# Kernel tuning notes

Measured on AMD Instinct MI355X. Metric: run time of the kernel, lower is better.

The kernel has to match this reference:

```python
import jax, jax.numpy as jnp
import numpy as np
import math

EPS = float(jnp.finfo(jnp.float32).eps)


def _mask_imag(z, n_ops):
    # Zero the imaginary part of (b,c) slices whose relative imaginary
    # magnitude is below the FFT roundoff threshold (vectorized version of
    # the original per-(i,j) Python loop).
    re, im = z.real, z.imag
    max_im = jnp.max(jnp.abs(im), axis=(-2, -1), keepdims=True)
    max_abs = jnp.max(jnp.abs(z), axis=(-2, -1), keepdims=True)
    mask = (max_im / max_abs) <= (n_ops * EPS)
    im = jnp.where(mask, jnp.zeros_like(im), im)
    return jax.lax.complex(re, im)


def otf2psf(otf, outsize):
    h, w = otf.shape[-2], otf.shape[-1]
    n_ops = h * w * (math.log2(h) + math.log2(w))
    psf = jnp.fft.ifft2(otf)
    psf = _mask_imag(psf, n_ops)
    psf = jnp.roll(psf, (outsize[0] // 2, outsize[1] // 2), axis=(-2, -1))
    return psf[..., : outsize[0], : outsize[1]]


def psf2otf(psf, shape):
    p0, p1 = psf.shape[-2], psf.shape[-1]
    n_ops = p0 * p1 * (math.log2(p0) + math.log2(p1))
    pad = [(0, 0)] * (psf.ndim - 2) + [(0, shape[0] - p0), (0, shape[1] - p1)]
    otf = jnp.pad(psf, pad)
    otf = jnp.roll(otf, (-(p0 // 2), -(p1 // 2)), axis=(-2, -1))
    otf = jnp.fft.fft2(otf)
    return _mask_imag(otf, n_ops)


def compute_ax(psf, latent_ft, image_size, psf_size_2d, gamma):
    xf = psf2otf(psf, image_size)          # [b, cp, H, W] complex
    y = jnp.real(otf2psf(latent_ft * xf, psf_size_2d))  # [b, c, p, p]
    return y + gamma * psf


def conjgrad(x, latent_ft, b_rhs, n_iter, image_size, psf_size_2d, gamma):
    r = b_rhs - compute_ax(x, latent_ft, image_size, psf_size_2d, gamma)
    p = r
    rsold = jnp.sum(r * r, axis=(-2, -1), keepdims=True)
    for _ in range(n_iter):  # small fixed iteration count
        Ap = compute_ax(p, latent_ft, image_size, psf_size_2d, gamma)
        alpha = rsold / jnp.sum(p * Ap, axis=(-2, -1), keepdims=True)
        x = x + alpha * p
        r = r - alpha * Ap
        rsnew = jnp.sum(r * r, axis=(-2, -1), keepdims=True)
        p = r + (rsnew / rsold) * p
        rsold = rsnew
    return x


def setup_inputs() -> dict:
    key = jax.random.key(0)
    k1, k2, k3, k4 = jax.random.split(key, 4)
    shape = (4, 3, 512, 512)
    return {
        "blurx": jax.random.normal(k1, shape, dtype=jnp.float32),
        "blury": jax.random.normal(k2, shape, dtype=jnp.float32),
        "latentx": jax.random.normal(k3, shape, dtype=jnp.float32),
        "latenty": jax.random.normal(k4, shape, dtype=jnp.float32),
        "psf_size": 31,
    }


def reference(blurx, blury, latentx, latenty, psf_size):
    n_iter = 10
    gamma = 1.0
    blur = jnp.sqrt(blurx ** 2 + blury ** 2)
    latent = jnp.sqrt(latentx ** 2 + latenty ** 2)
    b, c, h, w = blur.shape
    kernel = jnp.full((b, 1, psf_size, psf_size), 1.0 / float(psf_size ** 2), dtype=blur.dtype)
    blur_f = jnp.fft.fft2(blur)
    latent_f = jnp.fft.fft2(latent)
    bf = jnp.conj(latent_f) * blur_f
    latent_ft = jnp.conj(latent_f) * latent_f
    blur_otf = jnp.real(otf2psf(bf, (psf_size, psf_size)))  # [b, c, p, p]
    kernel = conjgrad(kernel, latent_ft, blur_otf, n_iter, (h, w), (psf_size, psf_size), gamma)
    # threshold small entries, clamp negatives, normalize
    kf = kernel.reshape(b, c, -1)
    max_var = jnp.max(kf, axis=2, keepdims=True)
    kf = jnp.where(kf < 0.05 * max_var, jnp.zeros_like(kf), kf)
    kernel = kf.reshape(b, c, psf_size, psf_size)
    kernel = jnp.where(kernel < 0, jnp.zeros_like(kernel), kernel)
    kernel = kernel / jnp.sum(kernel, axis=(-2, -1), keepdims=True)
    return kernel
```

## Files before the change

### kernel.cpp

```cpp
#include <hip/hip_runtime.h>
#include <math.h>

#define NIMG 12
#define NN 512
#define NPIX (NN * NN)
#define XST (257 * 512)

__device__ __forceinline__ int brev9(int p) {
  return (int)(__brev((unsigned)p) >> 23);
}

__device__ __forceinline__ void fft512_core(
    float vr[8], float vi[8], const int inv,
    const float* __restrict__ twr, const float* __restrict__ twi,
    const int lane)
{
#pragma unroll
  for (int s = 0; s < 3; ++s) {
    const int half = 1 << s;
#pragma unroll
    for (int e = 0; e < 8; ++e) {
      if ((e & half) == 0) {
        const int j = (e & (half - 1)) << (8 - s);
        const float wr = twr[j];
        const float wi = inv ? -twi[j] : twi[j];
        const float br = vr[e + half], bi = vi[e + half];
        const float tr = __fsub_rn(__fmul_rn(wr, br), __fmul_rn(wi, bi));
        const float ti = __fadd_rn(__fmul_rn(wr, bi), __fmul_rn(wi, br));
        vr[e + half] = __fsub_rn(vr[e], tr); vi[e + half] = __fsub_rn(vi[e], ti);
        vr[e] = __fadd_rn(vr[e], tr); vi[e] = __fadd_rn(vi[e], ti);
      }
    }
  }
#pragma unroll
  for (int s = 3; s <= 8; ++s) {
    const int xm = 1 << (s - 3);
    const bool low = (lane & xm) == 0;
#pragma unroll
    for (int e = 0; e < 8; ++e) {
      const float orr = __shfl_xor(vr[e], xm);
      const float oii = __shfl_xor(vi[e], xm);
      const int j = ((((lane & (xm - 1)) << 3) | e)) << (8 - s);
      const float wr = twr[j];
      const float wi = inv ? -twi[j] : twi[j];
      if (low) {
        const float tr = __fsub_rn(__fmul_rn(wr, orr), __fmul_rn(wi, oii));
        const float ti = __fadd_rn(__fmul_rn(wr, oii), __fmul_rn(wi, orr));
        vr[e] = __fadd_rn(vr[e], tr); vi[e] = __fadd_rn(vi[e], ti);
      } else {
        const float tr = __fsub_rn(__fmul_rn(wr, vr[e]), __fmul_rn(wi, vi[e]));
        const float ti = __fadd_rn(__fmul_rn(wr, vi[e]), __fmul_rn(wi, vr[e]));
        vr[e] = __fsub_rn(orr, tr); vi[e] = __fsub_rn(oii, ti);
      }
    }
  }
  if (inv) {
    const float sc = 1.0f / 512.0f;
#pragma unroll
    for (int e = 0; e < 8; ++e) {
      vr[e] = __fmul_rn(vr[e], sc); vi[e] = __fmul_rn(vi[e], sc);
    }
  }
}

__device__ __forceinline__ float np_pw_base(const float* a, int n)
{
  float r0 = a[0], r1 = a[1], r2 = a[2], r3 = a[3];
  float r4 = a[4], r5 = a[5], r6 = a[6], r7 = a[7];
  int i = 8;
  const int lim = n - (n & 7);
  for (; i < lim; i += 8) {
    r0 = __fadd_rn(r0, a[i + 0]); r1 = __fadd_rn(r1, a[i + 1]);
    r2 = __fadd_rn(r2, a[i + 2]); r3 = __fadd_rn(r3, a[i + 3]);
    r4 = __fadd_rn(r4, a[i + 4]); r5 = __fadd_rn(r5, a[i + 5]);
    r6 = __fadd_rn(r6, a[i + 6]); r7 = __fadd_rn(r7, a[i + 7]);
  }
  float res = __fadd_rn(
      __fadd_rn(__fadd_rn(r0, r1), __fadd_rn(r2, r3)),
      __fadd_rn(__fadd_rn(r4, r5), __fadd_rn(r6, r7)));
  for (; i < n; ++i) res = __fadd_rn(res, a[i]);
  return res;
}

__global__ __launch_bounds__(256) void twiddle_kernel(float2* __restrict__ twg)
{
  const int k = threadIdx.x;
  double s, c;
  sincos(-2.0 * M_PI * (double)k / 512.0, &s, &c);
  twg[k] = make_float2((float)c, (float)s);
}

__global__ __launch_bounds__(256) void loadmag_kernel(
    const float* __restrict__ bx, const float* __restrict__ by,
    const float* __restrict__ lx, const float* __restrict__ ly,
    float2* __restrict__ B2, float2* __restrict__ B1)
{
  const int i = blockIdx.x * 256 + threadIdx.x;
  {
    const float a = lx[i], b = ly[i];
    const float s = __fadd_rn(__fmul_rn(a, a), __fmul_rn(b, b));
    B2[i] = make_float2((float)sqrt((double)s), 0.f);
  }
  {
    const float a = bx[i], b = by[i];
    const float s = __fadd_rn(__fmul_rn(a, a), __fmul_rn(b, b));
    B1[i] = make_float2((float)sqrt((double)s), 0.f);
  }
}

__global__ __launch_bounds__(256) void rowfft_kernel(
    float2* __restrict__ A, float2* __restrict__ B,
    const float2* __restrict__ twg)
{
  __shared__ float twr[256], twi[256];
  { const float2 t = twg[threadIdx.x]; twr[threadIdx.x] = t.x; twi[threadIdx.x] = t.y; }
  __syncthreads();
  int wid = blockIdx.x * 4 + (threadIdx.x >> 6);
  const int lane = threadIdx.x & 63;
  float2* buf = A;
  if (wid >= NIMG * NN) { wid -= NIMG * NN; buf = B; }
  const int base = (wid >> 9) * NPIX + (wid & 511) * NN;
  float vr[8], vi[8];
#pragma unroll
  for (int e = 0; e < 8; ++e) {
    const float2 z = buf[base + brev9(lane * 8 + e)];
    vr[e] = z.x; vi[e] = z.y;
  }
  fft512_core(vr, vi, 0, twr, twi, lane);
#pragma unroll
  for (int e = 0; e < 8; ++e)
    buf[base + lane * 8 + e] = make_float2(vr[e], vi[e]);
}

__global__ __launch_bounds__(256) void colA_kernel(
    float2* __restrict__ B2, const float2* __restrict__ twg)
{
  __shared__ float twr[256], twi[256];
  __shared__ float2 ld[4][520];
  { const float2 t = twg[threadIdx.x]; twr[threadIdx.x] = t.x; twi[threadIdx.x] = t.y; }
  const int img = blockIdx.x >> 7;
  const int c0  = (blockIdx.x & 127) * 4;
  const int tid = threadIdx.x;
  float2* __restrict__ base = B2 + img * NPIX;
  for (int it = 0; it < 8; ++it) {
    const int idx = it * 256 + tid;
    ld[idx & 3][idx >> 2] = base[(idx >> 2) * NN + c0 + (idx & 3)];
  }
  __syncthreads();
  const int w = tid >> 6, lane = tid & 63;
  float vr[8], vi[8];
#pragma unroll
  for (int e = 0; e < 8; ++e) {
    const float2 z = ld[w][brev9(lane * 8 + e)];
    vr[e] = z.x; vi[e] = z.y;
  }
  fft512_core(vr, vi, 0, twr, twi, lane);
#pragma unroll
  for (int e = 0; e < 8; ++e) ld[w][lane * 8 + e] = make_float2(vr[e], vi[e]);
  __syncthreads();
  for (int it = 0; it < 8; ++it) {
    const int idx = it * 256 + tid;
    base[(idx >> 2) * NN + c0 + (idx & 3)] = ld[idx & 3][idx >> 2];
  }
}

__global__ __launch_bounds__(256) void colB_kernel(
    const float2* __restrict__ B1, float2* __restrict__ XH,
    const float2* __restrict__ twg)
{
  __shared__ float twr[256], twi[256];
  __shared__ float2 ld[4][520];
  { const float2 t = twg[threadIdx.x]; twr[threadIdx.x] = t.x; twi[threadIdx.x] = t.y; }
  const int img = blockIdx.x / 65;
  const int c0  = (blockIdx.x % 65) * 4;
  const int tid = threadIdx.x;
  const float2* __restrict__ in = B1 + img * NPIX;
  for (int it = 0; it < 8; ++it) {
    const int idx = it * 256 + tid;
    const int cc = c0 + (idx & 3);
    ld[idx & 3][idx >> 2] = in[(idx >> 2) * NN + (cc < NN ? cc : NN - 1)];
  }
  __syncthreads();
  const int w = tid >> 6, lane = tid & 63;
  const int c = c0 + w;
  if (c > 256) return;
  float vr[8], vi[8];
#pragma unroll
  for (int e = 0; e < 8; ++e) {
    const float2 z = ld[w][brev9(lane * 8 + e)];
    vr[e] = z.x; vi[e] = z.y;
  }
  fft512_core(vr, vi, 0, twr, twi, lane);
  float2* __restrict__ out = XH + (size_t)img * XST + c * NN + lane * 8;
#pragma unroll
  for (int e = 0; e < 8; ++e) out[e] = make_float2(vr[e], vi[e]);
}

__global__ __launch_bounds__(256) void fp_kernel(
    const float2* __restrict__ B2, float* __restrict__ FP)
{
  const int i = blockIdx.x * 256 + threadIdx.x;
  const float2 l = B2[i];
  FP[i] = __fadd_rn(__fmul_rn(l.x, l.x), __fmul_rn(l.y, l.y));
}

__global__ __launch_bounds__(256) void kb_kernel(
    const float2* __restrict__ R, float2* __restrict__ XH,
    unsigned* __restrict__ stats, const float2* __restrict__ twg)
{
  __shared__ float twr[256], twi[256];
  __shared__ float smi[4], sma[4];
  { const float2 t = twg[threadIdx.x]; twr[threadIdx.x] = t.x; twi[threadIdx.x] = t.y; }
  __syncthreads();
  const int img = blockIdx.x / 65;
  const int c   = (blockIdx.x % 65) * 4 + (threadIdx.x >> 6);
  const int lane = threadIdx.x & 63;
  float mi = 0.f, ma = 0.f;
  if (c <= 256) {
    float vr[8], vi[8];
#pragma unroll
    for (int e = 0; e < 8; ++e) {
      const int q = brev9(lane * 8 + e);
      const int k = (q + 15) & 511;
      if (k < 31) {
        const float2 z = R[(img * 31 + k) * NN + c];
        vr[e] = z.x; vi[e] = z.y;
      } else { vr[e] = 0.f; vi[e] = 0.f; }
    }
    fft512_core(vr, vi, 0, twr, twi, lane);
#pragma unroll
    for (int e = 0; e < 8; ++e) {
      mi = fmaxf(mi, fabsf(vi[e]));
      const float ab = (float)sqrt(
          (double)__fadd_rn(__fmul_rn(vr[e], vr[e]), __fmul_rn(vi[e], vi[e])));
      ma = fmaxf(ma, ab);
    }
    float2* __restrict__ out = XH + (size_t)img * XST + c * NN + lane * 8;
#pragma unroll
    for (int e = 0; e < 8; ++e) out[e] = make_float2(vr[e], vi[e]);
  }
#pragma unroll
  for (int off = 32; off; off >>= 1) {
    mi = fmaxf(mi, __shfl_xor(mi, off));
    ma = fmaxf(ma, __shfl_xor(ma, off));
  }
  if (lane == 0) { smi[threadIdx.x >> 6] = mi; sma[threadIdx.x >> 6] = ma; }
  __syncthreads();
  if (threadIdx.x == 0) {
    mi = fmaxf(fmaxf(smi[0], smi[1]), fmaxf(smi[2], smi[3]));
    ma = fmaxf(fmaxf(sma[0], sma[1]), fmaxf(sma[2], sma[3]));
    atomicMax(&stats[img * 2 + 0], __float_as_uint(mi));
    atomicMax(&stats[img * 2 + 1], __float_as_uint(ma));
  }
}

__global__ __launch_bounds__(256) void kprod_kernel(
    const float2* __restrict__ XH, const float2* __restrict__ B2,
    const float* __restrict__ FP, float2* __restrict__ Y,
    const unsigned* __restrict__ stats, const float2* __restrict__ twg,
    int bmode)
{
  __shared__ float twr[256], twi[256];
  __shared__ float2 T[8][257];
  { const float2 t = twg[threadIdx.x]; twr[threadIdx.x] = t.x; twi[threadIdx.x] = t.y; }
  const int img = blockIdx.x >> 6;
  const int g   = blockIdx.x & 63;
  const int tid = threadIdx.x;
  const float2* __restrict__ Xi = XH + (size_t)img * XST;
  for (int idx = tid; idx < 257 * 8; idx += 256) {
    const int c = idx >> 3, sub = idx & 7;
    int row;
    if (g == 0) row = (sub < 4) ? sub : ((sub < 7) ? (505 + sub) : 256);
    else        row = (sub < 4) ? (4 * g + sub) : (505 + sub - 4 * g);
    T[sub][c] = Xi[c * NN + row];
  }
  bool fire = false;
  if (bmode == 0) {
    const float m1 = __uint_as_float(stats[img * 2 + 0]);
    const float m2 = __uint_as_float(stats[img * 2 + 1]);
    const double MTHR =
        961.0 * (log2(31.0) + log2(31.0)) * 1.1920928955078125e-7;
    fire = ((double)__fdiv_rn(m1, m2) <= MTHR);
  }
  __syncthreads();
  const int w = tid >> 6, lane = tid & 63;
  for (int t = 0; t < 2; ++t) {
    const int oi = w + 4 * t;
    int r, slot_m;
    if (g == 0) {
      const int mir0[8] = {0, 6, 5, 4, 3, 2, 1, 7};
      r = (oi < 4) ? oi : ((oi < 7) ? (505 + oi) : 256);
      slot_m = mir0[oi];
    } else {
      r = (oi < 4) ? (4 * g + oi) : (505 + oi - 4 * g);
      slot_m = 7 - oi;
    }
    float vr[8], vi[8];
    if (bmode) {
      const float2* __restrict__ Lrow = B2 + img * NPIX + r * NN;
#pragma unroll
      for (int e = 0; e < 8; ++e) {
        const int q = brev9(lane * 8 + e);
        float2 xb;
        if (q <= 256) xb = T[oi][q];
        else { const float2 tt = T[slot_m][512 - q]; xb = make_float2(tt.x, -tt.y); }
        const float2 l = Lrow[q];
        vr[e] = __fadd_rn(__fmul_rn(l.x, xb.x), __fmul_rn(l.y, xb.y));
        vi[e] = __fsub_rn(__fmul_rn(l.x, xb.y), __fmul_rn(l.y, xb.x));
      }
    } else {
      const float* __restrict__ Frow = FP + img * NPIX + r * NN;
#pragma unroll
      for (int e = 0; e < 8; ++e) {
        const int q = brev9(lane * 8 + e);
        float2 xb;
        if (q <= 256) xb = T[oi][q];
        else { const float2 tt = T[slot_m][512 - q]; xb = make_float2(tt.x, -tt.y); }
        const float fi = fire ? 0.f : xb.y;
        const float F  = Frow[q];
        vr[e] = __fmul_rn(F, xb.x);
        vi[e] = __fmul_rn(F, fi);
      }
    }
    fft512_core(vr, vi, 1, twr, twi, lane);
#pragma unroll
    for (int e = 0; e < 8; ++e) {
      const int c2 = lane * 8 + e;
      if (c2 >= 497 || c2 <= 15) {
        const int v = (c2 + 15) & 511;
        Y[(img * 31 + v) * NN + r] = make_float2(vr[e], vi[e]);
      }
    }
  }
}

__global__ __launch_bounds__(256) void kA_kernel(
    const float2* __restrict__ Y, float* __restrict__ yv,
    const float2* __restrict__ twg)
{
  __shared__ float twr[256], twi[256];
  { const float2 t = twg[threadIdx.x]; twr[threadIdx.x] = t.x; twi[threadIdx.x] = t.y; }
  __syncthreads();
  const int wid = blockIdx.x * 4 + (threadIdx.x >> 6);
  if (wid >= NIMG * 31) return;
  const int lane = threadIdx.x & 63;
  const int img = wid / 31, v = wid - img * 31;
  const float2* __restrict__ Yv = Y + (img * 31 + v) * NN;
  float vr[8], vi[8];
#pragma unroll
  for (int e = 0; e < 8; ++e) {
    const float2 z = Yv[brev9(lane * 8 + e)];
    vr[e] = z.x; vi[e] = z.y;
  }
  fft512_core(vr, vi, 1, twr, twi, lane);
#pragma unroll
  for (int e = 0; e < 8; ++e) {
    const int q2 = lane * 8 + e;
    const int u = (q2 + 15) & 511;
    if (u < 31) yv[img * 961 + u * 31 + v] = vr[e];
  }
}

__global__ __launch_bounds__(1024) void kC_kernel(
    const float* __restrict__ yv, float2* __restrict__ R,
    float* __restrict__ bvec, float* __restrict__ xv,
    float* __restrict__ rv, float* __restrict__ pv,
    float* __restrict__ rsoldg, unsigned* __restrict__ stats,
    const float2* __restrict__ twg, float* __restrict__ out,
    int mode, int fin)
{
  __shared__ float twr[256], twi[256];
  __shared__ float pl[961], prodl[961];
  __shared__ float pwl[8], redf[16];
  __shared__ float scal;
  const int tid = threadIdx.x;
  const int wave = tid >> 6, lane = tid & 63;
  const int img = blockIdx.x;
  if (tid < 256) { const float2 t = twg[tid]; twr[tid] = t.x; twi[tid] = t.y; }
  __syncthreads();

  const bool act = tid < 961;
  const int g = img * 961 + tid;

  auto pairwise = [&]() -> float {
    __syncthreads();
    if (tid < 8) pwl[tid] = np_pw_base(prodl + tid * 120, (tid == 7) ? 121 : 120);
    __syncthreads();
    if (tid == 0) {
      const float L = __fadd_rn(__fadd_rn(pwl[0], pwl[1]), __fadd_rn(pwl[2], pwl[3]));
      const float Rr = __fadd_rn(__fadd_rn(pwl[4], pwl[5]), __fadd_rn(pwl[6], pwl[7]));
      scal = __fadd_rn(L, Rr);
    }
    __syncthreads();
    const float s = scal;
    __syncthreads();
    return s;
  };

  if (mode == 2) {
    if (act) {
      bvec[g] = yv[g];
      xv[g] = (float)(1.0 / 961.0);
      pl[tid] = (float)(1.0 / 961.0);
    }
  } else if (mode == 0) {
    if (act) {
      const float Ap = __fadd_rn(yv[g], xv[g]);
      const float r0 = __fsub_rn(bvec[g], Ap);
      rv[g] = r0; pv[g] = r0; pl[tid] = r0;
      prodl[tid] = __fmul_rn(r0, r0);
    }
    const float s = pairwise();
    if (tid == 0) rsoldg[img] = s;
  } else {
    float p = 0.f, Ap = 0.f, nr = 0.f;
    if (act) {
      p = pv[g];
      Ap = __fadd_rn(yv[g], p);
      prodl[tid] = __fmul_rn(p, Ap);
    }
    const float pAp = pairwise();
    if (tid == 0) scal = rsoldg[img] / pAp;
    __syncthreads();
    const float alpha = scal;
    __syncthreads();
    if (act) {
      xv[g] = __fadd_rn(xv[g], __fmul_rn(alpha, p));
      nr = __fsub_rn(rv[g], __fmul_rn(alpha, Ap));
      rv[g] = nr;
      prodl[tid] = __fmul_rn(nr, nr);
    }
    const float rsnew = pairwise();
    if (tid == 0) { scal = rsnew / rsoldg[img]; rsoldg[img] = rsnew; }
    __syncthreads();
    const float beta = scal;
    __syncthreads();
    if (act) {
      const float pn = __fadd_rn(nr, __fmul_rn(beta, p));
      pv[g] = pn; pl[tid] = pn;
    }
  }
  if (tid == 0) { stats[img * 2 + 0] = 0u; stats[img * 2 + 1] = 0u; }
  __syncthreads();

  if (fin) {
    const float x = act ? xv[g] : -3.4e38f;
    float v = x;
#pragma unroll
    for (int off = 32; off; off >>= 1) v = fmaxf(v, __shfl_xor(v, off));
    if (lane == 0) redf[wave] = v;
    __syncthreads();
    if (tid == 0) {
      float s = redf[0];
      for (int w2 = 1; w2 < 16; ++w2) s = fmaxf(s, redf[w2]);
      scal = s;
    }
    __syncthreads();
    const float maxv = scal;
    const float thrf = __fmul_rn(0.05f, maxv);
    float vvv = act ? x : 0.f;
    if (vvv < thrf) vvv = 0.f;
    if (vvv < 0.f)  vvv = 0.f;
    if (act) prodl[tid] = vvv;
    const float ssum = pairwise();
    if (act) out[g] = vvv / ssum;
    return;
  }

  for (int rep = 0; rep < 2; ++rep) {
    const int k = wave + 16 * rep;
    if (k < 31) {
      float vr[8], vi[8];
#pragma unroll
      for (int e = 0; e < 8; ++e) {
        const int q = brev9(lane * 8 + e);
        const int l = (q + 15) & 511;
        vr[e] = (l < 31) ? pl[k * 31 + l] : 0.f;
        vi[e] = 0.f;
      }
      fft512_core(vr, vi, 0, twr, twi, lane);
      float2* __restrict__ Rk = R + (img * 31 + k) * NN + lane * 8;
#pragma unroll
      for (int e = 0; e < 8; ++e) Rk[e] = make_float2(vr[e], vi[e]);
    }
  }
}

extern "C" void kernel_launch(void* const* d_in, const int* in_sizes, int n_in,
                              void* d_out, int out_size, void* d_ws, size_t ws_size,
                              hipStream_t stream)
{
  const float* bx = (const float*)d_in[0];
  const float* by = (const float*)d_in[1];
  const float* lx = (const float*)d_in[2];
  const float* ly = (const float*)d_in[3];

  float* ws = (float*)d_ws;
  float2* B1 = (float2*)ws;
  float2* B2 = B1 + (size_t)NIMG * NPIX;
  float2* XH = B2 + (size_t)NIMG * NPIX;
  float2* R  = XH + (size_t)NIMG * XST;
  float2* Y  = R  + (size_t)NIMG * 31 * NN;
  float*  FP = (float*)(Y + (size_t)NIMG * 31 * NN);
  float*  vec = FP + (size_t)NIMG * NPIX;
  float*  bvec = vec;
  float*  xv   = bvec + NIMG * 961;
  float*  rv   = xv   + NIMG * 961;
  float*  pv   = rv   + NIMG * 961;
  float*  yv   = pv   + NIMG * 961;
  float*  rsold = yv  + NIMG * 961;
  unsigned* stats = (unsigned*)(rsold + NIMG);
  float2* twg = (float2*)(stats + 24);
  float* out = (float*)d_out;

  twiddle_kernel<<<1, 256, 0, stream>>>(twg);
  loadmag_kernel<<<NIMG * NPIX / 256, 256, 0, stream>>>(bx, by, lx, ly, B2, B1);
  rowfft_kernel<<<2 * NIMG * NN / 4, 256, 0, stream>>>(B2, B1, twg);
  colA_kernel<<<NIMG * 128, 256, 0, stream>>>(B2, twg);
  colB_kernel<<<NIMG * 65, 256, 0, stream>>>(B1, XH, twg);
  fp_kernel<<<NIMG * NPIX / 256, 256, 0, stream>>>(B2, FP);
  kprod_kernel<<<NIMG * 64, 256, 0, stream>>>(XH, B2, FP, Y, stats, twg, 1);
  kA_kernel<<<(NIMG * 31 + 3) / 4, 256, 0, stream>>>(Y, yv, twg);
  kC_kernel<<<NIMG, 1024, 0, stream>>>(yv, R, bvec, xv, rv, pv, rsold, stats,
                                       twg, out, 2, 0);

  for (int a = 0; a < 11; ++a) {
    kb_kernel<<<NIMG * 65, 256, 0, stream>>>(R, XH, stats, twg);
    kprod_kernel<<<NIMG * 64, 256, 0, stream>>>(XH, B2, FP, Y, stats, twg, 0);
    kA_kernel<<<(NIMG * 31 + 3) / 4, 256, 0, stream>>>(Y, yv, twg);
    const int mode = (a == 0) ? 0 : 1;
    const int fin  = (a == 10) ? 1 : 0;
    kC_kernel<<<NIMG, 1024, 0, stream>>>(yv, R, bvec, xv, rv, pv, rsold, stats,
                                         twg, out, mode, fin);
  }
}
```

Before: 1.372 ms.

## Fuse power-spectrum into column FFT and permute XH rows for contiguous gather

The |F|^2 power spectrum is now computed and stored inside colA_kernel, which removes the separate fp_kernel launch and its extra read of B2. The column-FFT outputs in colB and kb are written in a permuted row order (rowslot) that places each row next to its mirror row. kprod can then gather its 8 rows per block as one contiguous span instead of two scattered groups. The trade-off is scattered writes in kb/colB and more complex index arithmetic.

```diff
diff --git a/kernel.cpp b/kernel.cpp
--- a/kernel.cpp
+++ b/kernel.cpp
@@ -8,6 +8,12 @@
 
 __device__ __forceinline__ int brev9(int p) {
   return (int)(__brev((unsigned)p) >> 23);
+}
+
+__device__ __forceinline__ int rowslot(int r) {
+  if (r == 0) return 0;
+  if (r == 256) return 1;
+  return (r < 256) ? (2 * r) : (2 * (512 - r) + 1);
 }
 
 __device__ __forceinline__ void fft512_core(
@@ -133,7 +139,8 @@
 }
 
 __global__ __launch_bounds__(256) void colA_kernel(
-    float2* __restrict__ B2, const float2* __restrict__ twg)
+    float2* __restrict__ B2, float* __restrict__ FP,
+    const float2* __restrict__ twg)
 {
   __shared__ float twr[256], twi[256];
   __shared__ float2 ld[4][520];
@@ -142,6 +149,7 @@
   const int c0  = (blockIdx.x & 127) * 4;
   const int tid = threadIdx.x;
   float2* __restrict__ base = B2 + img * NPIX;
+  float*  __restrict__ fpb  = FP + img * NPIX;
   for (int it = 0; it < 8; ++it) {
     const int idx = it * 256 + tid;
     ld[idx & 3][idx >> 2] = base[(idx >> 2) * NN + c0 + (idx & 3)];
@@ -160,7 +168,10 @@
   __syncthreads();
   for (int it = 0; it < 8; ++it) {
     const int idx = it * 256 + tid;
-    base[(idx >> 2) * NN + c0 + (idx & 3)] = ld[idx & 3][idx >> 2];
+    const float2 z = ld[idx & 3][idx >> 2];
+    const int off = (idx >> 2) * NN + c0 + (idx & 3);
+    base[off] = z;
+    fpb[off] = __fadd_rn(__fmul_rn(z.x, z.x), __fmul_rn(z.y, z.y));
   }
 }
 
@@ -191,17 +202,10 @@
     vr[e] = z.x; vi[e] = z.y;
   }
   fft512_core(vr, vi, 0, twr, twi, lane);
-  float2* __restrict__ out = XH + (size_t)img * XST + c * NN + lane * 8;
-#pragma unroll
-  for (int e = 0; e < 8; ++e) out[e] = make_float2(vr[e], vi[e]);
-}
-
-__global__ __launch_bounds__(256) void fp_kernel(
-    const float2* __restrict__ B2, float* __restrict__ FP)
-{
-  const int i = blockIdx.x * 256 + threadIdx.x;
-  const float2 l = B2[i];
-  FP[i] = __fadd_rn(__fmul_rn(l.x, l.x), __fmul_rn(l.y, l.y));
+  float2* __restrict__ out = XH + (size_t)img * XST + c * NN;
+#pragma unroll
+  for (int e = 0; e < 8; ++e)
+    out[rowslot(lane * 8 + e)] = make_float2(vr[e], vi[e]);
 }
 
 __global__ __launch_bounds__(256) void kb_kernel(
@@ -235,9 +239,10 @@
           (double)__fadd_rn(__fmul_rn(vr[e], vr[e]), __fmul_rn(vi[e], vi[e])));
       ma = fmaxf(ma, ab);
     }
-    float2* __restrict__ out = XH + (size_t)img * XST + c * NN + lane * 8;
-#pragma unroll
-    for (int e = 0; e < 8; ++e) out[e] = make_float2(vr[e], vi[e]);
+    float2* __restrict__ out = XH + (size_t)img * XST + c * NN;
+#pragma unroll
+    for (int e = 0; e < 8; ++e)
+      out[rowslot(lane * 8 + e)] = make_float2(vr[e], vi[e]);
   }
 #pragma unroll
   for (int off = 32; off; off >>= 1) {
@@ -269,10 +274,7 @@
   const float2* __restrict__ Xi = XH + (size_t)img * XST;
   for (int idx = tid; idx < 257 * 8; idx += 256) {
     const int c = idx >> 3, sub = idx & 7;
-    int row;
-    if (g == 0) row = (sub < 4) ? sub : ((sub < 7) ? (505 + sub) : 256);
-    else        row = (sub < 4) ? (4 * g + sub) : (505 + sub - 4 * g);
-    T[sub][c] = Xi[c * NN + row];
+    T[sub][c] = Xi[c * NN + 8 * g + sub];
   }
   bool fire = false;
   if (bmode == 0) {
@@ -286,15 +288,9 @@
   const int w = tid >> 6, lane = tid & 63;
   for (int t = 0; t < 2; ++t) {
     const int oi = w + 4 * t;
-    int r, slot_m;
-    if (g == 0) {
-      const int mir0[8] = {0, 6, 5, 4, 3, 2, 1, 7};
-      r = (oi < 4) ? oi : ((oi < 7) ? (505 + oi) : 256);
-      slot_m = mir0[oi];
-    } else {
-      r = (oi < 4) ? (4 * g + oi) : (505 + oi - 4 * g);
-      slot_m = 7 - oi;
-    }
+    const int r = (g == 0 && oi == 1) ? 256
+                : (((oi & 1) == 0) ? (4 * g + (oi >> 1)) : (512 - 4 * g - (oi >> 1)));
+    const int slot_m = (g == 0 && oi < 2) ? oi : (oi ^ 1);
     float vr[8], vi[8];
     if (bmode) {
       const float2* __restrict__ Lrow = B2 + img * NPIX + r * NN;
@@ -516,9 +512,8 @@
   twiddle_kernel<<<1, 256, 0, stream>>>(twg);
   loadmag_kernel<<<NIMG * NPIX / 256, 256, 0, stream>>>(bx, by, lx, ly, B2, B1);
   rowfft_kernel<<<2 * NIMG * NN / 4, 256, 0, stream>>>(B2, B1, twg);
-  colA_kernel<<<NIMG * 128, 256, 0, stream>>>(B2, twg);
+  colA_kernel<<<NIMG * 128, 256, 0, stream>>>(B2, FP, twg);
   colB_kernel<<<NIMG * 65, 256, 0, stream>>>(B1, XH, twg);
-  fp_kernel<<<NIMG * NPIX / 256, 256, 0, stream>>>(B2, FP);
   kprod_kernel<<<NIMG * 64, 256, 0, stream>>>(XH, B2, FP, Y, stats, twg, 1);
   kA_kernel<<<(NIMG * 31 + 3) / 4, 256, 0, stream>>>(Y, yv, twg);
   kC_kernel<<<NIMG, 1024, 0, stream>>>(yv, R, bvec, xv, rv, pv, rsold, stats,
```

Result: no change. 1.373 ms (+0.0%).
